# Kernel optimization log

Measured on AMD Instinct MI355X. Metric: run time of the kernel, lower is better.

Reference implementation:

```python
import jax, jax.numpy as jnp
import numpy as np

N = 4096  # size of every layer (I, H1, H2, O)
EPS = 1e-5  # torch LayerNorm default


def _ln(x, g, b):
    # torch.nn.LayerNorm: biased variance, affine
    mu = jnp.mean(x)
    xc = x - mu
    v = jnp.mean(xc * xc)
    return xc * jax.lax.rsqrt(v + EPS) * g + b


def setup_inputs() -> dict:
    key = jax.random.key(0)
    ks = jax.random.split(key, 24)
    W = 0.02  # weight scale ~ uniform-init magnitude of nn.Linear at fan_in=4096
    inp = {
        "input_raw": jax.random.normal(ks[0], (N,), jnp.float32),
        "h1_prev": jax.random.normal(ks[1], (N,), jnp.float32),
        "h2_prev": jax.random.normal(ks[2], (N,), jnp.float32),
        "W_I_H1": jax.random.normal(ks[3], (N, N), jnp.float32) * W,
        "W_H1_H1": jax.random.normal(ks[4], (N, N), jnp.float32) * W,
        "W_H1_H2": jax.random.normal(ks[5], (N, N), jnp.float32) * W,
        "W_H2_H1": jax.random.normal(ks[6], (N, N), jnp.float32) * W,
        "W_H2_H2": jax.random.normal(ks[7], (N, N), jnp.float32) * W,
        "W_H1_O": jax.random.normal(ks[8], (N, N), jnp.float32) * W,
        "W_H2_O": jax.random.normal(ks[9], (N, N), jnp.float32) * W,
        "bias_h1": jax.random.normal(ks[10], (N,), jnp.float32) * 0.1,
        "bias_h2": jax.random.normal(ks[11], (N,), jnp.float32) * 0.1,
        "bias_o": jax.random.normal(ks[12], (N,), jnp.float32) * 0.1,
        "g_i": jax.random.uniform(ks[13], (N,), jnp.float32, 0.5, 1.5),
        "b_i": jax.random.normal(ks[14], (N,), jnp.float32) * 0.1,
        "g_h1": jax.random.uniform(ks[15], (N,), jnp.float32, 0.5, 1.5),
        "bln_h1": jax.random.normal(ks[16], (N,), jnp.float32) * 0.1,
        "g_h2": jax.random.uniform(ks[17], (N,), jnp.float32, 0.5, 1.5),
        "bln_h2": jax.random.normal(ks[18], (N,), jnp.float32) * 0.1,
        "g_o": jax.random.uniform(ks[19], (N,), jnp.float32, 0.5, 1.5),
        "bln_o": jax.random.normal(ks[20], (N,), jnp.float32) * 0.1,
    }
    return inp


def reference(input_raw, h1_prev, h2_prev,
              W_I_H1, W_H1_H1, W_H1_H2, W_H2_H1, W_H2_H2, W_H1_O, W_H2_O,
              bias_h1, bias_h2, bias_o,
              g_i, b_i, g_h1, bln_h1, g_h2, bln_h2, g_o, bln_o):
    # --- Phase 1: feedback accumulation + per-layer LayerNorm ---
    # I and O have no feedback -> LN(zeros) = LN bias (beta)
    i_out = b_i + input_raw                       # layers['I']: LN(0) then += input_raw
    h1_fb = _ln(W_H1_H1 @ h1_prev, g_h1, bln_h1)  # self-recurrent feedback H1->H1
    h2_fb = _ln(W_H2_H2 @ h2_prev, g_h2, bln_h2)  # self-recurrent feedback H2->H2
    o_init = bln_o                                # layers['O']: LN(zeros)

    # --- Phase 2: input-driven / feedback-only hidden activations ---
    h1_p2 = jax.nn.relu(_ln(W_I_H1 @ i_out + h1_fb + bias_h1, g_h1, bln_h1))  # 'I' in forward
    h2_p2 = jax.nn.relu(_ln(h2_fb + bias_h2, g_h2, bln_h2))                    # feedback-only

    # --- Phase 3: inter-hidden forward pass (intermediate_output OVERWRITES) ---
    h1_f = jax.nn.relu(_ln(W_H2_H1 @ h2_p2 + bias_h1, g_h1, bln_h1))
    h2_f = jax.nn.relu(_ln(W_H1_H2 @ h1_p2 + bias_h2, g_h2, bln_h2))

    # --- Output layer: sum forwards, tanh(LN(.)) ---
    o = jnp.tanh(_ln(o_init + W_H1_O @ h1_f + W_H2_O @ h2_f + bias_o, g_o, bln_o))
    return o
```

## Files before the change

### kernel.cpp

```cpp
#include <hip/hip_runtime.h>
#include <math.h>

#define NN 4096
#define ROWS_PER_BLOCK 16
#define GX 256
#define BLK 256


__device__ __forceinline__ float4 ld4(const float* __restrict__ p, int t) {
    return reinterpret_cast<const float4*>(p)[t];
}
__device__ __forceinline__ void st4(float* __restrict__ p, int t, float4 v) {
    reinterpret_cast<float4*>(p)[t] = v;
}
__device__ __forceinline__ float4 add4(float4 a, float4 b) {
    return make_float4(a.x + b.x, a.y + b.y, a.z + b.z, a.w + b.w);
}

typedef const __attribute__((address_space(1))) unsigned int* gas1_u32;
typedef __attribute__((address_space(3))) unsigned int* las3_u32;
template<int AUX>
__device__ __forceinline__ void async16(const float* g, float* l) {
    __builtin_amdgcn_global_load_lds((gas1_u32)(const void*)g, (las3_u32)(void*)l, 16, 0, AUX);
}

template<int AUX>
__device__ __forceinline__ void stage_row(const float* __restrict__ W, int row,
                                          float* __restrict__ buf, int wave, int lane) {
    const float* g = W + (size_t)row * NN + wave * 1024 + lane * 4;
    float* l = buf + wave * 1024;
    async16<AUX>(g,       l);
    async16<AUX>(g + 256, l + 256);
    async16<AUX>(g + 512, l + 512);
    async16<AUX>(g + 768, l + 768);
}

__device__ __forceinline__ float dot_row(const float* __restrict__ buf,
                                         const float4 xr[4], int tid) {
    const float4* b4 = reinterpret_cast<const float4*>(buf);
    float p = 0.f;
    #pragma unroll
    for (int i = 0; i < 4; ++i) {
        float4 w = b4[i * 256 + tid];
        p = fmaf(w.x, xr[i].x, p);
        p = fmaf(w.y, xr[i].y, p);
        p = fmaf(w.z, xr[i].z, p);
        p = fmaf(w.w, xr[i].w, p);
    }
    #pragma unroll
    for (int off = 32; off > 0; off >>= 1) p += __shfl_down(p, off, 64);
    return p;
}

__device__ __forceinline__ float2 block_reduce2(float s, float ss, float* sbuf) {
    #pragma unroll
    for (int off = 32; off > 0; off >>= 1) {
        s  += __shfl_down(s,  off, 64);
        ss += __shfl_down(ss, off, 64);
    }
    const int wave = threadIdx.x >> 6;
    const int lane = threadIdx.x & 63;
    if (lane == 0) { sbuf[wave] = s; sbuf[16 + wave] = ss; }
    __syncthreads();
    float rs = 0.f, rss = 0.f;
    if (threadIdx.x < 16) { rs = sbuf[threadIdx.x]; rss = sbuf[16 + threadIdx.x]; }
    if (wave == 0) {
        #pragma unroll
        for (int off = 8; off > 0; off >>= 1) {
            rs  += __shfl_down(rs,  off, 64);
            rss += __shfl_down(rss, off, 64);
        }
        if (lane == 0) { sbuf[0] = rs; sbuf[1] = rss; }
    }
    __syncthreads();
    float2 r = make_float2(sbuf[0], sbuf[1]);
    __syncthreads();
    return r;
}

struct LNStat { float mu, rstd; };

__device__ __forceinline__ LNStat ln_stats(float4 v, float* sbuf) {
    float s  = v.x + v.y + v.z + v.w;
    float ss = v.x * v.x + v.y * v.y + v.z * v.z + v.w * v.w;
    float2 r = block_reduce2(s, ss, sbuf);
    LNStat o;
    o.mu = r.x * (1.0f / NN);
    float var = r.y * (1.0f / NN) - o.mu * o.mu;
    o.rstd = rsqrtf(var + 1e-5f);
    return o;
}

__device__ __forceinline__ float4 ln_apply(float4 v, LNStat st, float4 g, float4 b) {
    return make_float4((v.x - st.mu) * st.rstd * g.x + b.x,
                       (v.y - st.mu) * st.rstd * g.y + b.y,
                       (v.z - st.mu) * st.rstd * g.z + b.z,
                       (v.w - st.mu) * st.rstd * g.w + b.w);
}

__device__ __forceinline__ float4 relu4(float4 v) {
    return make_float4(fmaxf(v.x, 0.f), fmaxf(v.y, 0.f), fmaxf(v.z, 0.f), fmaxf(v.w, 0.f));
}


template<int AUX>
__device__ __forceinline__ void gemv_core(const float* __restrict__ W,
                                          const float* __restrict__ x,
                                          const float* __restrict__ xadd,
                                          float* __restrict__ y,
                                          float* t0, float* t1, float* sbuf) {
    const int tid  = threadIdx.x;
    const int wave = tid >> 6;
    const int lane = tid & 63;
    const int r0 = blockIdx.x;

    stage_row<AUX>(W, r0, t0, wave, lane);

    float4 xr[4];
    const float4* x4 = reinterpret_cast<const float4*>(x);
    #pragma unroll
    for (int i = 0; i < 4; ++i) xr[i] = x4[i * 256 + tid];
    if (xadd) {
        const float4* a4 = reinterpret_cast<const float4*>(xadd);
        #pragma unroll
        for (int i = 0; i < 4; ++i) xr[i] = add4(xr[i], a4[i * 256 + tid]);
    }
    __syncthreads();

    #pragma unroll 1
    for (int j = 0; j < ROWS_PER_BLOCK; j += 2) {
        if (tid == 0 && j > 0) y[r0 + (j - 1) * GX] = sbuf[4] + sbuf[5] + sbuf[6] + sbuf[7];
        if (j + 1 < ROWS_PER_BLOCK) stage_row<AUX>(W, r0 + (j + 1) * GX, t1, wave, lane);
        {
            float p = dot_row(t0, xr, tid);
            if (lane == 0) sbuf[wave] = p;
        }
        __syncthreads();
        if (tid == 0) y[r0 + j * GX] = sbuf[0] + sbuf[1] + sbuf[2] + sbuf[3];
        if (j + 2 < ROWS_PER_BLOCK) stage_row<AUX>(W, r0 + (j + 2) * GX, t0, wave, lane);
        {
            float p = dot_row(t1, xr, tid);
            if (lane == 0) sbuf[4 + wave] = p;
        }
        __syncthreads();
    }
    if (tid == 0) y[r0 + (ROWS_PER_BLOCK - 1) * GX] = sbuf[4] + sbuf[5] + sbuf[6] + sbuf[7];
}

__global__ __launch_bounds__(BLK) void gemv_stageA(
    const float* __restrict__ W_H1_H1, const float* __restrict__ h1_prev,
    const float* __restrict__ W_H2_H2, const float* __restrict__ h2_prev,
    const float* __restrict__ W_I_H1,  const float* __restrict__ input_raw,
    const float* __restrict__ b_i,
    float* __restrict__ mv1, float* __restrict__ mv2, float* __restrict__ mv3)
{
    __shared__ float t0[NN], t1[NN];
    __shared__ float sbuf[8];
    const float* W; const float* x; const float* xadd; float* y;
    if (blockIdx.y == 0)      { W = W_H1_H1; x = h1_prev;   xadd = nullptr; y = mv1; }
    else if (blockIdx.y == 1) { W = W_H2_H2; x = h2_prev;   xadd = nullptr; y = mv2; }
    else                      { W = W_I_H1;  x = input_raw; xadd = b_i;     y = mv3; }
    gemv_core<2>(W, x, xadd, y, t0, t1, sbuf);
}

__global__ __launch_bounds__(BLK) void gemv_pair(
    const float* __restrict__ Wa, const float* __restrict__ xa, float* __restrict__ ya,
    const float* __restrict__ Wb, const float* __restrict__ xb, float* __restrict__ yb)
{
    __shared__ float t0[NN], t1[NN];
    __shared__ float sbuf[8];
    const float* W; const float* x; float* y;
    if (blockIdx.y == 0) { W = Wa; x = xa; y = ya; }
    else                 { W = Wb; x = xb; y = yb; }
    gemv_core<0>(W, x, nullptr, y, t0, t1, sbuf);
}

__global__ __launch_bounds__(1024) void phase2_kernel(
    const float* __restrict__ mv1, const float* __restrict__ mv2, const float* __restrict__ mv3,
    const float* __restrict__ bias_h1, const float* __restrict__ bias_h2,
    const float* __restrict__ g_h1, const float* __restrict__ bln_h1,
    const float* __restrict__ g_h2, const float* __restrict__ bln_h2,
    float* __restrict__ h1_p2, float* __restrict__ h2_p2)
{
    __shared__ float sbuf[32];
    const int t = threadIdx.x;
    if (blockIdx.x == 0) {
        float4 g = ld4(g_h1, t), b = ld4(bln_h1, t);
        float4 v = ld4(mv1, t);
        LNStat s1 = ln_stats(v, sbuf);
        float4 fb = ln_apply(v, s1, g, b);
        float4 tt = add4(add4(ld4(mv3, t), fb), ld4(bias_h1, t));
        LNStat s2 = ln_stats(tt, sbuf);
        st4(h1_p2, t, relu4(ln_apply(tt, s2, g, b)));
    } else {
        float4 g = ld4(g_h2, t), b = ld4(bln_h2, t);
        float4 v = ld4(mv2, t);
        LNStat s1 = ln_stats(v, sbuf);
        float4 fb = ln_apply(v, s1, g, b);
        float4 tt = add4(fb, ld4(bias_h2, t));
        LNStat s2 = ln_stats(tt, sbuf);
        st4(h2_p2, t, relu4(ln_apply(tt, s2, g, b)));
    }
}

__global__ __launch_bounds__(1024) void phase3_kernel(
    const float* __restrict__ mv4, const float* __restrict__ mv5,
    const float* __restrict__ bias_h1, const float* __restrict__ bias_h2,
    const float* __restrict__ g_h1, const float* __restrict__ bln_h1,
    const float* __restrict__ g_h2, const float* __restrict__ bln_h2,
    float* __restrict__ h1_f, float* __restrict__ h2_f)
{
    __shared__ float sbuf[32];
    const int t = threadIdx.x;
    const float* mv;  const float* bias; const float* g; const float* b; float* out;
    if (blockIdx.x == 0) { mv = mv4; bias = bias_h1; g = g_h1; b = bln_h1; out = h1_f; }
    else                 { mv = mv5; bias = bias_h2; g = g_h2; b = bln_h2; out = h2_f; }
    float4 v = add4(ld4(mv, t), ld4(bias, t));
    LNStat s = ln_stats(v, sbuf);
    st4(out, t, relu4(ln_apply(v, s, ld4(g, t), ld4(b, t))));
}

__global__ __launch_bounds__(1024) void final_kernel(
    const float* __restrict__ mv6, const float* __restrict__ mv7,
    const float* __restrict__ bias_o, const float* __restrict__ bln_o,
    const float* __restrict__ g_o,
    float* __restrict__ out)
{
    __shared__ float sbuf[32];
    const int t = threadIdx.x;
    float4 v = add4(add4(ld4(bln_o, t), ld4(mv6, t)), add4(ld4(mv7, t), ld4(bias_o, t)));
    LNStat s = ln_stats(v, sbuf);
    float4 r = ln_apply(v, s, ld4(g_o, t), ld4(bln_o, t));
    st4(out, t, make_float4(tanhf(r.x), tanhf(r.y), tanhf(r.z), tanhf(r.w)));
}


extern "C" void kernel_launch(void* const* d_in, const int* in_sizes, int n_in,
                              void* d_out, int out_size, void* d_ws, size_t ws_size,
                              hipStream_t stream) {
    const float* input_raw = (const float*)d_in[0];
    const float* h1_prev   = (const float*)d_in[1];
    const float* h2_prev   = (const float*)d_in[2];
    const float* W_I_H1    = (const float*)d_in[3];
    const float* W_H1_H1   = (const float*)d_in[4];
    const float* W_H1_H2   = (const float*)d_in[5];
    const float* W_H2_H1   = (const float*)d_in[6];
    const float* W_H2_H2   = (const float*)d_in[7];
    const float* W_H1_O    = (const float*)d_in[8];
    const float* W_H2_O    = (const float*)d_in[9];
    const float* bias_h1   = (const float*)d_in[10];
    const float* bias_h2   = (const float*)d_in[11];
    const float* bias_o    = (const float*)d_in[12];
    const float* b_i       = (const float*)d_in[14];
    const float* g_h1      = (const float*)d_in[15];
    const float* bln_h1    = (const float*)d_in[16];
    const float* g_h2      = (const float*)d_in[17];
    const float* bln_h2    = (const float*)d_in[18];
    const float* g_o       = (const float*)d_in[19];
    const float* bln_o     = (const float*)d_in[20];

    float* ws    = (float*)d_ws;
    float* mv1   = ws;
    float* mv2   = ws + 1 * NN;
    float* mv3   = ws + 2 * NN;
    float* h1_p2 = ws + 3 * NN;
    float* h2_p2 = ws + 4 * NN;
    float* mv4   = ws + 5 * NN;
    float* mv5   = ws + 6 * NN;
    float* h1_f  = ws + 7 * NN;
    float* h2_f  = ws + 8 * NN;
    float* mv6   = ws + 9 * NN;
    float* mv7   = ws + 10 * NN;

    gemv_stageA<<<dim3(GX, 3), BLK, 0, stream>>>(
        W_H1_H1, h1_prev, W_H2_H2, h2_prev, W_I_H1, input_raw, b_i, mv1, mv2, mv3);

    phase2_kernel<<<2, 1024, 0, stream>>>(
        mv1, mv2, mv3, bias_h1, bias_h2, g_h1, bln_h1, g_h2, bln_h2, h1_p2, h2_p2);

    gemv_pair<<<dim3(GX, 2), BLK, 0, stream>>>(
        W_H2_H1, h2_p2, mv4, W_H1_H2, h1_p2, mv5);

    phase3_kernel<<<2, 1024, 0, stream>>>(
        mv4, mv5, bias_h1, bias_h2, g_h1, bln_h1, g_h2, bln_h2, h1_f, h2_f);

    gemv_pair<<<dim3(GX, 2), BLK, 0, stream>>>(
        W_H1_O, h1_f, mv6, W_H2_O, h2_f, mv7);

    final_kernel<<<1, 1024, 0, stream>>>(
        mv6, mv7, bias_o, bln_o, g_o, (float*)d_out);
}
```

Before: 86.87 us.

## Triple-buffer GEMV row staging with explicit vmcnt waits and unrolled loop

Moves the GEMV core from double to triple-buffered LDS row tiles, so two rows are in flight while the current row is dotted. It swaps __syncthreads for explicit s_waitcnt vmcnt(4) plus s_barrier, which waits only for the oldest async load batch. Per-row results now collect in shared memory and are written out together at the end rather than by thread 0 each step. LDS use rises from 32KB to 48KB per block, which may reduce occupancy, and the hand-counted vmcnt values depend on how many loads stage_row issues.

```diff
diff --git a/kernel.cpp b/kernel.cpp
--- a/kernel.cpp
+++ b/kernel.cpp
@@ -2,8 +2,8 @@
 #include <math.h>
 
 #define NN 4096
-#define ROWS_PER_BLOCK 16
 #define GX 256
+#define NROWS 16
 #define BLK 256
 
 
@@ -108,13 +108,11 @@
                                           const float* __restrict__ x,
                                           const float* __restrict__ xadd,
                                           float* __restrict__ y,
-                                          float* t0, float* t1, float* sbuf) {
+                                          float* tiles, float* sbuf, float* ys) {
     const int tid  = threadIdx.x;
     const int wave = tid >> 6;
     const int lane = tid & 63;
     const int r0 = blockIdx.x;
-
-    stage_row<AUX>(W, r0, t0, wave, lane);
 
     float4 xr[4];
     const float4* x4 = reinterpret_cast<const float4*>(x);
@@ -125,26 +123,37 @@
         #pragma unroll
         for (int i = 0; i < 4; ++i) xr[i] = add4(xr[i], a4[i * 256 + tid]);
     }
+    asm volatile("s_waitcnt vmcnt(0)" ::: "memory");
+
+    stage_row<AUX>(W, r0 + 0 * GX, tiles + 0 * NN, wave, lane);
+    stage_row<AUX>(W, r0 + 1 * GX, tiles + 1 * NN, wave, lane);
+    asm volatile("s_waitcnt vmcnt(4)" ::: "memory");
+    __builtin_amdgcn_sched_barrier(0);
+    __builtin_amdgcn_s_barrier();
+
+    #pragma unroll
+    for (int j = 0; j < NROWS; ++j) {
+        if (tid == 0 && j > 0) {
+            const int pp = ((j - 1) & 1) * 4;
+            ys[j - 1] = sbuf[pp] + sbuf[pp + 1] + sbuf[pp + 2] + sbuf[pp + 3];
+        }
+        if (j + 2 < NROWS)
+            stage_row<AUX>(W, r0 + (j + 2) * GX, tiles + ((j + 2) % 3) * NN, wave, lane);
+        float p = dot_row(tiles + (j % 3) * NN, xr, tid);
+        if (lane == 0) sbuf[(j & 1) * 4 + wave] = p;
+        if (j <= NROWS - 3)
+            asm volatile("s_waitcnt vmcnt(4) lgkmcnt(0)" ::: "memory");
+        else
+            asm volatile("s_waitcnt vmcnt(0) lgkmcnt(0)" ::: "memory");
+        __builtin_amdgcn_sched_barrier(0);
+        __builtin_amdgcn_s_barrier();
+    }
+    if (tid == 0) {
+        const int pp = ((NROWS - 1) & 1) * 4;
+        ys[NROWS - 1] = sbuf[pp] + sbuf[pp + 1] + sbuf[pp + 2] + sbuf[pp + 3];
+    }
     __syncthreads();
-
-    #pragma unroll 1
-    for (int j = 0; j < ROWS_PER_BLOCK; j += 2) {
-        if (tid == 0 && j > 0) y[r0 + (j - 1) * GX] = sbuf[4] + sbuf[5] + sbuf[6] + sbuf[7];
-        if (j + 1 < ROWS_PER_BLOCK) stage_row<AUX>(W, r0 + (j + 1) * GX, t1, wave, lane);
-        {
-            float p = dot_row(t0, xr, tid);
-            if (lane == 0) sbuf[wave] = p;
-        }
-        __syncthreads();
-        if (tid == 0) y[r0 + j * GX] = sbuf[0] + sbuf[1] + sbuf[2] + sbuf[3];
-        if (j + 2 < ROWS_PER_BLOCK) stage_row<AUX>(W, r0 + (j + 2) * GX, t0, wave, lane);
-        {
-            float p = dot_row(t1, xr, tid);
-            if (lane == 0) sbuf[4 + wave] = p;
-        }
-        __syncthreads();
-    }
-    if (tid == 0) y[r0 + (ROWS_PER_BLOCK - 1) * GX] = sbuf[4] + sbuf[5] + sbuf[6] + sbuf[7];
+    if (tid < NROWS) y[r0 + tid * GX] = ys[tid];
 }
 
 __global__ __launch_bounds__(BLK) void gemv_stageA(
@@ -154,25 +163,27 @@
     const float* __restrict__ b_i,
     float* __restrict__ mv1, float* __restrict__ mv2, float* __restrict__ mv3)
 {
-    __shared__ float t0[NN], t1[NN];
+    __shared__ float tiles[3 * NN];
     __shared__ float sbuf[8];
+    __shared__ float ys[NROWS];
     const float* W; const float* x; const float* xadd; float* y;
     if (blockIdx.y == 0)      { W = W_H1_H1; x = h1_prev;   xadd = nullptr; y = mv1; }
     else if (blockIdx.y == 1) { W = W_H2_H2; x = h2_prev;   xadd = nullptr; y = mv2; }
     else                      { W = W_I_H1;  x = input_raw; xadd = b_i;     y = mv3; }
-    gemv_core<2>(W, x, xadd, y, t0, t1, sbuf);
+    gemv_core<2>(W, x, xadd, y, tiles, sbuf, ys);
 }
 
 __global__ __launch_bounds__(BLK) void gemv_pair(
     const float* __restrict__ Wa, const float* __restrict__ xa, float* __restrict__ ya,
     const float* __restrict__ Wb, const float* __restrict__ xb, float* __restrict__ yb)
 {
-    __shared__ float t0[NN], t1[NN];
+    __shared__ float tiles[3 * NN];
     __shared__ float sbuf[8];
+    __shared__ float ys[NROWS];
     const float* W; const float* x; float* y;
     if (blockIdx.y == 0) { W = Wa; x = xa; y = ya; }
     else                 { W = Wb; x = xb; y = yb; }
-    gemv_core<0>(W, x, nullptr, y, t0, t1, sbuf);
+    gemv_core<0>(W, x, nullptr, y, tiles, sbuf, ys);
 }
 
 __global__ __launch_bounds__(1024) void phase2_kernel(
```

After: 92.88 us. +6.9%, slower.
